# Kernel optimization log

Hardware: AMD Instinct MI355X
Metric: run time of the kernel (lower is better)

The kernel has to match this reference:

```python
import jax, jax.numpy as jnp
import numpy as np
import math

D_MODEL = 1024
N_HEADS = 16
D_HEAD = D_MODEL // N_HEADS
NUM_BUCKETS = 32
MAX_DISTANCE = 128


def _relative_position_bucket(relative_position):
    # bidirectional T5-style bucketing
    num_buckets = NUM_BUCKETS // 2
    buckets = (relative_position > 0).astype(jnp.int32) * num_buckets
    rp = jnp.abs(relative_position)
    max_exact = num_buckets // 2
    is_small = rp < max_exact
    rpf = jnp.maximum(rp, 1).astype(jnp.float32)  # avoid log(0); masked by is_small
    rp_large = max_exact + (
        jnp.log(rpf / max_exact) / math.log(MAX_DISTANCE / max_exact) * (num_buckets - max_exact)
    ).astype(jnp.int32)
    rp_large = jnp.minimum(rp_large, num_buckets - 1)
    return buckets + jnp.where(is_small, rp, rp_large)


def _compute_bias(q_len, k_len, rel_emb):
    context_pos = jnp.arange(q_len, dtype=jnp.int32)[:, None]
    memory_pos = jnp.arange(k_len, dtype=jnp.int32)[None, :]
    rp_bucket = _relative_position_bucket(memory_pos - context_pos)  # [Tq, Tk]
    values = rel_emb[rp_bucket]                 # [Tq, Tk, H]
    return jnp.transpose(values, (2, 0, 1))[None]  # [1, H, Tq, Tk]


def setup_inputs() -> dict:
    key = jax.random.key(0)
    ks = jax.random.split(key, 8)
    B, T = 4, 2048
    return {
        "query": jax.random.normal(ks[0], (B, T, D_MODEL), dtype=jnp.float32),
        "key": jax.random.normal(ks[1], (B, T, D_MODEL), dtype=jnp.float32),
        "value": jax.random.normal(ks[2], (B, T, D_MODEL), dtype=jnp.float32),
        "Wq": jax.random.normal(ks[3], (D_MODEL, D_MODEL), dtype=jnp.float32) * 0.02,
        "Wk": jax.random.normal(ks[4], (D_MODEL, D_MODEL), dtype=jnp.float32) * 0.02,
        "Wv": jax.random.normal(ks[5], (D_MODEL, D_MODEL), dtype=jnp.float32) * 0.02,
        "Wo": jax.random.normal(ks[6], (D_MODEL, D_MODEL), dtype=jnp.float32) * 0.02,
        "rel_emb": jax.random.normal(ks[7], (NUM_BUCKETS, N_HEADS), dtype=jnp.float32) * 0.02,
    }


def reference(query, key, value, Wq, Wk, Wv, Wo, rel_emb):
    B, Tq, _ = query.shape
    Tk = key.shape[1]
    # torch nn.Linear(bias=False): y = x @ W.T
    q = (query @ Wq.T).reshape(B, Tq, N_HEADS, D_HEAD).transpose(0, 2, 1, 3)  # [B,H,Tq,Dh]
    k = (key @ Wk.T).reshape(B, Tk, N_HEADS, D_HEAD).transpose(0, 2, 1, 3)
    v = (value @ Wv.T).reshape(B, Tk, N_HEADS, D_HEAD).transpose(0, 2, 1, 3)
    scores = jnp.einsum("bhqd,bhkd->bhqk", q, k) / math.sqrt(D_HEAD)  # [B,H,Tq,Tk]
    position_bias = _compute_bias(Tq, Tk, rel_emb)
    scores = scores + position_bias
    attn = jax.nn.softmax(scores, axis=-1)
    out = jnp.einsum("bhqk,bhkd->bhqd", attn, v)
    out = out.transpose(0, 2, 1, 3).reshape(B, Tq, D_MODEL)
    out = out @ Wo.T
    return out, position_bias
```

## Files before the change

### kernel.cpp

```cpp
#include <hip/hip_runtime.h>

typedef _Float16 half8 __attribute__((ext_vector_type(8)));
typedef _Float16 half4 __attribute__((ext_vector_type(4)));
typedef float f32x4 __attribute__((ext_vector_type(4)));

#define DEV __device__ __forceinline__

DEV f32x4 mfma16(half8 a, half8 b, f32x4 c) {
  return __builtin_amdgcn_mfma_f32_16x16x32_f16(a, b, c, 0, 0, 0);
}

DEV void load_lds16(const void* g, void* l) {
  __builtin_amdgcn_global_load_lds((const __attribute__((address_space(1))) void*)g,
                                   (__attribute__((address_space(3))) void*)l, 16, 0, 0);
}

DEV int t5_bucket(int delta) {
  int b = (delta > 0) ? 16 : 0;
  int rp = delta < 0 ? -delta : delta;
  if (rp < 8) return b + rp;
  float lg = logf((float)rp * 0.125f);
  int large = 8 + (int)(lg / 2.772588722239781f * 8.0f);
  if (large > 15) large = 15;
  return b + large;
}

DEV float bias_val(const float* rel, int n, int h) {
  return rel[t5_bucket(n - 2047) * 16 + h];
}

__global__ __launch_bounds__(256) void prep_kernel(
    const float* __restrict__ q, const float* __restrict__ k, const float* __restrict__ v,
    const float* __restrict__ wq, const float* __restrict__ wk, const float* __restrict__ wv,
    const float* __restrict__ wo, const float* __restrict__ rel,
    _Float16* __restrict__ Xh, _Float16* __restrict__ W3h, _Float16* __restrict__ Woh,
    _Float16* __restrict__ BiasH, float* __restrict__ Bf) {
  unsigned u = blockIdx.x * 256u + threadIdx.x;
  if (u < 6291456u) {
    unsigned p = u / 2097152u, r = u - p * 2097152u;
    const float4* s = (const float4*)(p == 0 ? q : p == 1 ? k : v);
    float4 x = s[r];
    half4 hv = {(_Float16)x.x, (_Float16)x.y, (_Float16)x.z, (_Float16)x.w};
    *(half4*)(Xh + (size_t)p * 8388608u + (size_t)r * 4u) = hv;
  } else if (u < 7340032u) {
    unsigned t = u - 6291456u;
    const float4* s;
    _Float16* d;
    if (t < 786432u) {
      unsigned p = t / 262144u, r = t - p * 262144u;
      s = (const float4*)(p == 0 ? wq : p == 1 ? wk : wv) + r;
      d = W3h + (size_t)p * 1048576u + (size_t)r * 4u;
    } else {
      unsigned r = t - 786432u;
      s = (const float4*)wo + r;
      d = Woh + (size_t)r * 4u;
    }
    float4 x = *s;
    half4 hv = {(_Float16)x.x, (_Float16)x.y, (_Float16)x.z, (_Float16)x.w};
    *(half4*)d = hv;
  } else {
    unsigned t = u - 7340032u;
    int h = (int)(t >> 12), n = (int)(t & 4095u);
    Bf[h * 4096 + n] = (n <= 4094) ? bias_val(rel, n, h) : 0.f;
    half4 hv;
#pragma unroll
    for (int j = 0; j < 4; j++) {
      float bv = (n + j <= 4094) ? bias_val(rel, n + j, h) * 1.4426950408889634f : 0.f;
      hv[j] = (_Float16)bv;
    }
    *(half4*)(BiasH + (size_t)(h * 4096 + n) * 4u) = hv;
  }
}

template <int MODE>
__global__ __launch_bounds__(256) void gemm128(
    const _Float16* __restrict__ A, const _Float16* __restrict__ B,
    _Float16* __restrict__ D0, _Float16* __restrict__ D1, _Float16* __restrict__ D2,
    float* __restrict__ F) {
  __shared__ _Float16 Asm[128 * 64];
  __shared__ _Float16 Bsm[128 * 64];
  const int tid = threadIdx.x;
  const int w = tid >> 6, L = tid & 63;
  const int g = L >> 4, c15 = L & 15;
  const int m0 = blockIdx.x * 128, n0 = blockIdx.y * 128;
  const int z = blockIdx.z;
  const _Float16* Ab = A + ((size_t)z * 8192 + m0) * 1024;
  const _Float16* Bb = B + ((size_t)z * 1024 + n0) * 1024;
  f32x4 acc[4][4] = {};
  const int mw = (w & 1) * 64, nw = (w >> 1) * 64;
  const int wbase = tid & ~63;
  for (int k0 = 0; k0 < 1024; k0 += 64) {
    __syncthreads();
#pragma unroll
    for (int c = 0; c < 4; c++) {
      int i = c * 256 + tid;
      int row = i >> 3, pc = i & 7;
      int lc = pc ^ ((row >> 1) & 7);
      load_lds16(Ab + (size_t)row * 1024 + k0 + lc * 8, Asm + (c * 256 + wbase) * 8);
      load_lds16(Bb + (size_t)row * 1024 + k0 + lc * 8, Bsm + (c * 256 + wbase) * 8);
    }
    __builtin_amdgcn_s_waitcnt(0);
    __syncthreads();
#pragma unroll
    for (int kc = 0; kc < 2; kc++) {
      half8 af[4], bf[4];
#pragma unroll
      for (int t = 0; t < 4; t++) {
        int rowA = mw + t * 16 + c15;
        int pcA = (kc * 4 + g) ^ ((rowA >> 1) & 7);
        af[t] = *(const half8*)(Asm + rowA * 64 + pcA * 8);
        int rowB = nw + t * 16 + c15;
        int pcB = (kc * 4 + g) ^ ((rowB >> 1) & 7);
        bf[t] = *(const half8*)(Bsm + rowB * 64 + pcB * 8);
      }
#pragma unroll
      for (int mt = 0; mt < 4; mt++)
#pragma unroll
        for (int nt = 0; nt < 4; nt++)
          acc[mt][nt] = mfma16(bf[nt], af[mt], acc[mt][nt]);
    }
  }
  if (MODE == 0) {
    float scale = (z == 0) ? 0.18033688011112042f : 1.0f;
    _Float16* dst = (z == 0) ? D0 : (z == 1) ? D1 : D2;
#pragma unroll
    for (int mt = 0; mt < 4; mt++) {
      int m = m0 + mw + mt * 16 + c15;
      int bb = m >> 11, t = m & 2047;
#pragma unroll
      for (int nt = 0; nt < 4; nt++) {
        int n = n0 + nw + nt * 16 + g * 4;
        half4 hv;
#pragma unroll
        for (int r = 0; r < 4; r++) hv[r] = (_Float16)(acc[mt][nt][r] * scale);
        *(half4*)(dst + (((size_t)bb * 16 + (n >> 6)) * 2048 + t) * 64 + (n & 63)) = hv;
      }
    }
  } else {
#pragma unroll
    for (int mt = 0; mt < 4; mt++) {
      int m = m0 + mw + mt * 16 + c15;
#pragma unroll
      for (int nt = 0; nt < 4; nt++) {
        int n = n0 + nw + nt * 16 + g * 4;
        float4 fv = make_float4(acc[mt][nt][0], acc[mt][nt][1], acc[mt][nt][2], acc[mt][nt][3]);
        *(float4*)(F + (size_t)m * 1024 + n) = fv;
      }
    }
  }
}

__global__ __launch_bounds__(256) void transpose_v(const _Float16* __restrict__ V,
                                                   _Float16* __restrict__ Vt) {
  int bh = blockIdx.z * 16 + blockIdx.y;
  const _Float16* Vb = V + (size_t)bh * 2048 * 64;
  _Float16* Vtb = Vt + (size_t)bh * 64 * 2048;
  int tid = threadIdx.x;
  __shared__ _Float16 tileS[64][64];
  int t0 = blockIdx.x * 64;
#pragma unroll
  for (int c = 0; c < 2; c++) {
    int i = c * 256 + tid;
    int row = i >> 3, col = (i & 7) * 8;
    half8 vv = *(const half8*)(Vb + (size_t)(t0 + row) * 64 + col);
    int xr = 8 * ((col >> 3) & 7);
#pragma unroll
    for (int j = 0; j < 8; j++) tileS[col + j][row ^ xr] = vv[j];
  }
  __syncthreads();
  int d = tid >> 2, c = (tid & 3) * 16;
  int xr = 8 * ((d >> 3) & 7);
  half8 o0 = *(const half8*)(&tileS[d][c ^ xr]);
  half8 o1 = *(const half8*)(&tileS[d][(c + 8) ^ xr]);
  *(half8*)(Vtb + (size_t)d * 2048 + t0 + c) = o0;
  *(half8*)(Vtb + (size_t)d * 2048 + t0 + c + 8) = o1;
}

__global__ __launch_bounds__(256, 2) void flash_attn(
    const _Float16* __restrict__ Q, const _Float16* __restrict__ K,
    const _Float16* __restrict__ Vt, const _Float16* __restrict__ BiasH,
    _Float16* __restrict__ AO) {
  __shared__ _Float16 Kst[2][64 * 64];
  __shared__ _Float16 Vst[2][64 * 64];
  __shared__ half4 biasS[2304];
  __shared__ _Float16 pS[4][64][40];
  const int b = blockIdx.z, h = blockIdx.x, qb = blockIdx.y * 256;
  const int bh = b * 16 + h;
  const _Float16* Qb = Q + (size_t)bh * 2048 * 64;
  const _Float16* Kb = K + (size_t)bh * 2048 * 64;
  const _Float16* Vtb = Vt + (size_t)bh * 64 * 2048;
  const int tid = threadIdx.x, w = tid >> 6, L = tid & 63;
  const int g = L >> 4, c15 = L & 15;
  const int wbase = tid & ~63;
  const int idx0 = 1792 - qb;

  auto stage = [&](int buf, int kk) {
#pragma unroll
    for (int c = 0; c < 2; c++) {
      int i = c * 256 + tid;
      int row = i >> 3, pc = i & 7, lc = pc ^ ((row >> 1) & 7);
      load_lds16(Kb + (size_t)(kk + row) * 64 + lc * 8, &Kst[buf][(c * 256 + wbase) * 8]);
    }
#pragma unroll
    for (int c = 0; c < 2; c++) {
      int i = c * 256 + tid;
      int row = i >> 3, pc = i & 7, lc = pc ^ ((row >> 1) & 7);
      load_lds16(Vtb + (size_t)row * 2048 + kk + lc * 8, &Vst[buf][(c * 256 + wbase) * 8]);
    }
  };

  stage(0, 0);
  for (int i = tid; i < 2304; i += 256)
    biasS[i] = *(const half4*)(BiasH + (size_t)(h * 4096 + idx0 + i) * 4u);
  half8 qf[4][2];
#pragma unroll
  for (int r2 = 0; r2 < 4; r2++)
#pragma unroll
    for (int kc = 0; kc < 2; kc++)
      qf[r2][kc] =
          *(const half8*)(Qb + (size_t)(qb + w * 64 + r2 * 16 + c15) * 64 + kc * 32 + g * 8);
  f32x4 O[4][4] = {};
  float lsum[4] = {0.f, 0.f, 0.f, 0.f};
  __builtin_amdgcn_s_waitcnt(0);
  __syncthreads();

  for (int kt = 0; kt < 32; kt++) {
    const int cur = kt & 1, nxt = cur ^ 1;
    if (kt < 31) stage(nxt, (kt + 1) * 64);
#pragma unroll
    for (int p = 0; p < 2; p++) {
      half8 kf[2][2];
#pragma unroll
      for (int nt2 = 0; nt2 < 2; nt2++)
#pragma unroll
        for (int kc = 0; kc < 2; kc++) {
          int row = (2 * p + nt2) * 16 + c15;
          int pc = (kc * 4 + g) ^ ((row >> 1) & 7);
          kf[nt2][kc] = *(const half8*)(&Kst[cur][row * 64 + pc * 8]);
        }
      half8 vf[4];
#pragma unroll
      for (int dt = 0; dt < 4; dt++) {
        int row = dt * 16 + c15;
        int pc = (p * 4 + g) ^ ((row >> 1) & 7);
        vf[dt] = *(const half8*)(&Vst[cur][row * 64 + pc * 8]);
      }
#pragma unroll
      for (int r2 = 0; r2 < 4; r2++) {
        int qloc = w * 64 + r2 * 16 + c15;
#pragma unroll
        for (int nt2 = 0; nt2 < 2; nt2++) {
          f32x4 z = {};
          f32x4 s0 = mfma16(kf[nt2][0], qf[r2][0], z);
          f32x4 S = mfma16(kf[nt2][1], qf[r2][1], s0);
          half4 bv = biasS[kt * 64 + p * 32 + nt2 * 16 + g * 4 + 255 - qloc];
          half4 pv;
          float e0 = __builtin_amdgcn_exp2f(S[0] + (float)bv[0]);
          float e1 = __builtin_amdgcn_exp2f(S[1] + (float)bv[1]);
          float e2 = __builtin_amdgcn_exp2f(S[2] + (float)bv[2]);
          float e3 = __builtin_amdgcn_exp2f(S[3] + (float)bv[3]);
          lsum[r2] += (e0 + e1) + (e2 + e3);
          pv[0] = (_Float16)e0;
          pv[1] = (_Float16)e1;
          pv[2] = (_Float16)e2;
          pv[3] = (_Float16)e3;
          *(half4*)(&pS[w][r2 * 16 + c15][nt2 * 16 + g * 4]) = pv;
        }
      }
      __builtin_amdgcn_s_waitcnt(0xc07f);
      half8 pa[4];
#pragma unroll
      for (int r2 = 0; r2 < 4; r2++) pa[r2] = *(const half8*)(&pS[w][r2 * 16 + c15][g * 8]);
      __builtin_amdgcn_s_setprio(1);
#pragma unroll
      for (int r2 = 0; r2 < 4; r2++)
#pragma unroll
        for (int dt = 0; dt < 4; dt++) O[r2][dt] = mfma16(vf[dt], pa[r2], O[r2][dt]);
      __builtin_amdgcn_s_setprio(0);
    }
    __builtin_amdgcn_s_waitcnt(0);
    __syncthreads();
  }
#pragma unroll
  for (int r2 = 0; r2 < 4; r2++) {
    float ls = lsum[r2];
    ls += __shfl_xor(ls, 16, 64);
    ls += __shfl_xor(ls, 32, 64);
    float linv = 1.0f / ls;
    int qg = qb + w * 64 + r2 * 16 + c15;
    _Float16* dst = AO + ((size_t)(b * 2048 + qg)) * 1024 + h * 64;
#pragma unroll
    for (int dt = 0; dt < 4; dt++) {
      half4 ov;
#pragma unroll
      for (int r = 0; r < 4; r++) ov[r] = (_Float16)(O[r2][dt][r] * linv);
      *(half4*)(dst + dt * 16 + g * 4) = ov;
    }
  }
}

__global__ __launch_bounds__(256) void bias_out_k(const float* __restrict__ Bf,
                                                  float4* __restrict__ out2) {
  unsigned u = blockIdx.x * 256u + threadIdx.x;
  int hh = (int)(u >> 20);
  unsigned rem = u & 1048575u;
  int i = (int)(rem >> 9);
  int j4 = (int)(rem & 511u) * 4;
  const float* p = Bf + hh * 4096 + j4 - i + 2047;
  out2[u] = make_float4(p[0], p[1], p[2], p[3]);
}

extern "C" void kernel_launch(void* const* d_in, const int* in_sizes, int n_in,
                              void* d_out, int out_size, void* d_ws, size_t ws_size,
                              hipStream_t stream) {
  const float* q = (const float*)d_in[0];
  const float* k = (const float*)d_in[1];
  const float* v = (const float*)d_in[2];
  const float* wq = (const float*)d_in[3];
  const float* wk = (const float*)d_in[4];
  const float* wv = (const float*)d_in[5];
  const float* wo = (const float*)d_in[6];
  const float* rel = (const float*)d_in[7];

  _Float16* Xh = (_Float16*)d_ws;
  _Float16* W3h = Xh + 3u * 8388608u;
  _Float16* Woh = W3h + 3u * 1048576u;
  _Float16* Qh = Woh + 1048576u;
  _Float16* Kh = Qh + 8388608u;
  _Float16* Vh = Kh + 8388608u;
  _Float16* Vth = Vh + 8388608u;
  _Float16* AOh = Vth + 8388608u;
  _Float16* BiasH = AOh + 8388608u;
  float* Bf = (float*)(BiasH + 262144u);
  float* outp = (float*)d_out;

  prep_kernel<<<28928, 256, 0, stream>>>(q, k, v, wq, wk, wv, wo, rel, Xh, W3h, Woh, BiasH, Bf);
  gemm128<0><<<dim3(64, 8, 3), 256, 0, stream>>>(Xh, W3h, Qh, Kh, Vh, nullptr);
  transpose_v<<<dim3(32, 16, 4), 256, 0, stream>>>(Vh, Vth);
  flash_attn<<<dim3(16, 8, 4), 256, 0, stream>>>(Qh, Kh, Vth, BiasH, AOh);
  gemm128<1><<<dim3(64, 8, 1), 256, 0, stream>>>(AOh, Woh, nullptr, nullptr, nullptr, outp);
  bias_out_k<<<65536, 256, 0, stream>>>(Bf, (float4*)(outp + 8388608u));
}
```

Baseline: 601.9 us.

## Split flash attention over two key halves and combine partial outputs

Flash attention now splits the key range into two halves per block, doubling the grid from 512 to 1024 blocks. Each half writes unnormalized fp32 partial outputs and row sums, and a new combine kernel adds them and normalizes. This works without max-rescaling because the softmax uses no running max. The bias LDS table is dropped in favour of direct global loads, which frees shared memory so launch bounds can rise to 3 blocks per CU. The aim is to fill the GPU better, at the cost of extra fp32 partial traffic and one more kernel launch.

```diff
diff --git a/kernel.cpp b/kernel.cpp
--- a/kernel.cpp
+++ b/kernel.cpp
@@ -176,15 +176,15 @@
   *(half8*)(Vtb + (size_t)d * 2048 + t0 + c + 8) = o1;
 }
 
-__global__ __launch_bounds__(256, 2) void flash_attn(
+__global__ __launch_bounds__(256, 3) void flash_attn(
     const _Float16* __restrict__ Q, const _Float16* __restrict__ K,
     const _Float16* __restrict__ Vt, const _Float16* __restrict__ BiasH,
-    _Float16* __restrict__ AO) {
+    float* __restrict__ Op, float* __restrict__ Lp) {
   __shared__ _Float16 Kst[2][64 * 64];
   __shared__ _Float16 Vst[2][64 * 64];
-  __shared__ half4 biasS[2304];
   __shared__ _Float16 pS[4][64][40];
-  const int b = blockIdx.z, h = blockIdx.x, qb = blockIdx.y * 256;
+  const int b = blockIdx.z >> 1, kh = blockIdx.z & 1;
+  const int h = blockIdx.x, qb = blockIdx.y * 256;
   const int bh = b * 16 + h;
   const _Float16* Qb = Q + (size_t)bh * 2048 * 64;
   const _Float16* Kb = K + (size_t)bh * 2048 * 64;
@@ -193,6 +193,8 @@
   const int g = L >> 4, c15 = L & 15;
   const int wbase = tid & ~63;
   const int idx0 = 1792 - qb;
+  const _Float16* Bp =
+      BiasH + (size_t)(h * 4096 + idx0 + 255 + g * 4 - w * 64 - c15) * 4;
 
   auto stage = [&](int buf, int kk) {
 #pragma unroll
@@ -209,9 +211,7 @@
     }
   };
 
-  stage(0, 0);
-  for (int i = tid; i < 2304; i += 256)
-    biasS[i] = *(const half4*)(BiasH + (size_t)(h * 4096 + idx0 + i) * 4u);
+  stage(0, kh * 1024);
   half8 qf[4][2];
 #pragma unroll
   for (int r2 = 0; r2 < 4; r2++)
@@ -224,11 +224,19 @@
   __builtin_amdgcn_s_waitcnt(0);
   __syncthreads();
 
-  for (int kt = 0; kt < 32; kt++) {
-    const int cur = kt & 1, nxt = cur ^ 1;
-    if (kt < 31) stage(nxt, (kt + 1) * 64);
+  for (int kt2 = 0; kt2 < 16; kt2++) {
+    const int akt = kh * 16 + kt2;
+    const int cur = kt2 & 1, nxt = cur ^ 1;
+    if (kt2 < 15) stage(nxt, (akt + 1) * 64);
 #pragma unroll
     for (int p = 0; p < 2; p++) {
+      half4 bvv[4][2];
+#pragma unroll
+      for (int r2 = 0; r2 < 4; r2++)
+#pragma unroll
+        for (int nt2 = 0; nt2 < 2; nt2++)
+          bvv[r2][nt2] =
+              *(const half4*)(Bp + (ptrdiff_t)(akt * 64 + p * 32 + (nt2 - r2) * 16) * 4);
       half8 kf[2][2];
 #pragma unroll
       for (int nt2 = 0; nt2 < 2; nt2++)
@@ -238,22 +246,14 @@
           int pc = (kc * 4 + g) ^ ((row >> 1) & 7);
           kf[nt2][kc] = *(const half8*)(&Kst[cur][row * 64 + pc * 8]);
         }
-      half8 vf[4];
-#pragma unroll
-      for (int dt = 0; dt < 4; dt++) {
-        int row = dt * 16 + c15;
-        int pc = (p * 4 + g) ^ ((row >> 1) & 7);
-        vf[dt] = *(const half8*)(&Vst[cur][row * 64 + pc * 8]);
-      }
 #pragma unroll
       for (int r2 = 0; r2 < 4; r2++) {
-        int qloc = w * 64 + r2 * 16 + c15;
 #pragma unroll
         for (int nt2 = 0; nt2 < 2; nt2++) {
           f32x4 z = {};
           f32x4 s0 = mfma16(kf[nt2][0], qf[r2][0], z);
           f32x4 S = mfma16(kf[nt2][1], qf[r2][1], s0);
-          half4 bv = biasS[kt * 64 + p * 32 + nt2 * 16 + g * 4 + 255 - qloc];
+          half4 bv = bvv[r2][nt2];
           half4 pv;
           float e0 = __builtin_amdgcn_exp2f(S[0] + (float)bv[0]);
           float e1 = __builtin_amdgcn_exp2f(S[1] + (float)bv[1]);
@@ -267,6 +267,13 @@
           *(half4*)(&pS[w][r2 * 16 + c15][nt2 * 16 + g * 4]) = pv;
         }
       }
+      half8 vf[4];
+#pragma unroll
+      for (int dt = 0; dt < 4; dt++) {
+        int row = dt * 16 + c15;
+        int pc = (p * 4 + g) ^ ((row >> 1) & 7);
+        vf[dt] = *(const half8*)(&Vst[cur][row * 64 + pc * 8]);
+      }
       __builtin_amdgcn_s_waitcnt(0xc07f);
       half8 pa[4];
 #pragma unroll
@@ -281,22 +288,40 @@
     __builtin_amdgcn_s_waitcnt(0);
     __syncthreads();
   }
+  float* Opb = Op + ((size_t)(kh * 64 + bh) * 2048) * 64;
 #pragma unroll
   for (int r2 = 0; r2 < 4; r2++) {
     float ls = lsum[r2];
     ls += __shfl_xor(ls, 16, 64);
     ls += __shfl_xor(ls, 32, 64);
-    float linv = 1.0f / ls;
     int qg = qb + w * 64 + r2 * 16 + c15;
-    _Float16* dst = AO + ((size_t)(b * 2048 + qg)) * 1024 + h * 64;
+    if (g == 0) Lp[(size_t)(kh * 64 + bh) * 2048 + qg] = ls;
 #pragma unroll
     for (int dt = 0; dt < 4; dt++) {
-      half4 ov;
-#pragma unroll
-      for (int r = 0; r < 4; r++) ov[r] = (_Float16)(O[r2][dt][r] * linv);
-      *(half4*)(dst + dt * 16 + g * 4) = ov;
-    }
-  }
+      float4 fv = make_float4(O[r2][dt][0], O[r2][dt][1], O[r2][dt][2], O[r2][dt][3]);
+      *(float4*)(Opb + (size_t)qg * 64 + dt * 16 + g * 4) = fv;
+    }
+  }
+}
+
+__global__ __launch_bounds__(256) void combine_k(const float* __restrict__ Op,
+                                                 const float* __restrict__ Lp,
+                                                 _Float16* __restrict__ AO) {
+  unsigned u = blockIdx.x * 256u + threadIdx.x;
+  int d4 = (int)(u & 15u);
+  unsigned bq = u >> 4;
+  int bh = (int)(bq >> 11), qq = (int)(bq & 2047u);
+  const float4* A = (const float4*)Op + (size_t)bq * 16 + d4;
+  const float4* B = A + 2097152u;
+  float linv = 1.0f / (Lp[bq] + Lp[131072u + bq]);
+  float4 a = *A, c = *B;
+  half4 o;
+  o[0] = (_Float16)((a.x + c.x) * linv);
+  o[1] = (_Float16)((a.y + c.y) * linv);
+  o[2] = (_Float16)((a.z + c.z) * linv);
+  o[3] = (_Float16)((a.w + c.w) * linv);
+  int b_ = bh >> 4, h = bh & 15;
+  *(half4*)(AO + ((size_t)(b_ * 2048 + qq)) * 1024 + h * 64 + d4 * 4) = o;
 }
 
 __global__ __launch_bounds__(256) void bias_out_k(const float* __restrict__ Bf,
@@ -332,12 +357,15 @@
   _Float16* AOh = Vth + 8388608u;
   _Float16* BiasH = AOh + 8388608u;
   float* Bf = (float*)(BiasH + 262144u);
+  float* Opart = Bf + 262144u;
+  float* Lpart = Opart + 16777216u;
   float* outp = (float*)d_out;
 
   prep_kernel<<<28928, 256, 0, stream>>>(q, k, v, wq, wk, wv, wo, rel, Xh, W3h, Woh, BiasH, Bf);
   gemm128<0><<<dim3(64, 8, 3), 256, 0, stream>>>(Xh, W3h, Qh, Kh, Vh, nullptr);
   transpose_v<<<dim3(32, 16, 4), 256, 0, stream>>>(Vh, Vth);
-  flash_attn<<<dim3(16, 8, 4), 256, 0, stream>>>(Qh, Kh, Vth, BiasH, AOh);
+  flash_attn<<<dim3(16, 8, 8), 256, 0, stream>>>(Qh, Kh, Vth, BiasH, Opart, Lpart);
+  combine_k<<<8192, 256, 0, stream>>>(Opart, Lpart, AOh);
   gemm128<1><<<dim3(64, 8, 1), 256, 0, stream>>>(AOh, Woh, nullptr, nullptr, nullptr, outp);
   bias_out_k<<<65536, 256, 0, stream>>>(Bf, (float4*)(outp + 8388608u));
 }
```

Measured after the change: 681.6 us. +13.3%, slower.
